# Optimization experiments

Measured on AMD Instinct MI355X. Metric: run time of the kernel, lower is better.

Reference implementation:

```python
import jax, jax.numpy as jnp
import numpy as np

B = 4096          # batch of samples
M = 128           # n_orbitals
F = 32            # n_fermions
H = 512           # hidden_units


def setup_inputs() -> dict:
    key = jax.random.key(0)
    kn, kphi, kw1, kb1, kw2, kb2 = jax.random.split(key, 6)
    # occupancy strings: exactly F ones among M orbitals per sample
    keys = jax.random.split(kn, B)
    occ_idx = jax.vmap(lambda k: jax.random.permutation(k, M)[:F])(keys)  # [B,F]
    n = jnp.zeros((B, M), jnp.float32).at[jnp.arange(B)[:, None], occ_idx].set(1.0)
    # parameters
    Phi = jax.random.normal(kphi, (F, M), jnp.float32) * 0.1
    W1 = jax.random.normal(kw1, (M, H), jnp.float32) / np.sqrt(M)
    b1 = jnp.zeros((H,), jnp.float32)
    W2 = jax.random.normal(kw2, (H, F * M), jnp.float32) / np.sqrt(H)
    b2 = jnp.zeros((F * M,), jnp.float32)
    return {"n": n, "Phi": Phi, "W1": W1, "b1": b1, "W2": W2, "b2": b2}


def reference(n, Phi, W1, b1, W2, b2):
    # backflow MLP: Dense -> tanh -> Dense, reshaped to (F, M) per sample
    h = jnp.tanh(n @ W1 + b1)                       # [B,H]
    bf = (h @ W2 + b2).reshape(-1, F, M)            # [B,F,M]
    kernel = Phi[None] + bf                         # [B,F,M]
    # occupied orbital columns; exactly F ones per row, top_k is stable so
    # indices come out in ascending order (same as jnp.where(n, size=F))
    idx = jax.lax.top_k(n, F)[1]                    # [B,F] int32
    phi = jnp.take_along_axis(kernel, idx[:, None, :], axis=2)  # [B,F,F]
    sign, logabs = jnp.linalg.slogdet(phi)
    return jnp.log(sign.astype(jnp.complex64)) + logabs.astype(jnp.complex64)  # [B] complex
```

## Files before the change

kernel.cpp:

```cpp
#include <hip/hip_runtime.h>
#include <hip/hip_bf16.h>
#include <math.h>

#define B_N 4096
#define M_N 128
#define F_N 32
#define H_N 512
#define NFM 4096

#define WAVE_SYNC() do { \
  asm volatile("s_waitcnt lgkmcnt(0)" ::: "memory"); \
  __builtin_amdgcn_sched_barrier(0); \
} while (0)

__global__ __launch_bounds__(256) void k1_idx_h(
    const float* __restrict__ n, const float* __restrict__ W1,
    const float* __restrict__ b1, float* __restrict__ h_ws,
    unsigned int* __restrict__ mask)
{
  __shared__ int s_idx[F_N];
  __shared__ int s_cnt0;
  const int b = blockIdx.x;
  const int t = threadIdx.x;

  bool p = false;
  int before = 0;
  if (t < 128) {
    float v = n[(size_t)b * M_N + t];
    p = v > 0.5f;
    unsigned long long m = __ballot(p);
    int lane = t & 63;
    before = __popcll(m & ((1ull << lane) - 1ull));
    if (lane == 0) {
      if (t < 64) { mask[b*4+0] = (unsigned)m; mask[b*4+1] = (unsigned)(m>>32); }
      else        { mask[b*4+2] = (unsigned)m; mask[b*4+3] = (unsigned)(m>>32); }
    }
    if (t < 64) {
      if (lane == 0) s_cnt0 = __popcll(m);
      if (p) s_idx[before] = t;
    }
  }
  __syncthreads();
  if (t >= 64 && t < 128 && p) s_idx[s_cnt0 + before] = t;
  __syncthreads();

  #pragma unroll
  for (int cc = 0; cc < 2; ++cc) {
    int c = t + cc * 256;
    float acc = 0.0f;
    #pragma unroll
    for (int j = 0; j < F_N; ++j)
      acc += W1[(size_t)s_idx[j] * H_N + c];
    acc += b1[c];
    h_ws[(size_t)b * H_N + c] = tanhf(acc);
  }
}

__global__ __launch_bounds__(256) void k_w2t(
    const float* __restrict__ W2, float* __restrict__ W2t)
{
  __shared__ float lds[32 * 132];
  const int k = blockIdx.x;
  const int t = threadIdx.x;

  #pragma unroll
  for (int i = 0; i < 4; ++i) {
    int m0 = i * 1024 + t * 4;
    float4 v = *(const float4*)&W2[(size_t)k * NFM + m0];
    int ig = m0 >> 7, c = m0 & 127;
    lds[ig * 132 + c + 0] = v.x;
    lds[ig * 132 + c + 1] = v.y;
    lds[ig * 132 + c + 2] = v.z;
    lds[ig * 132 + c + 3] = v.w;
  }
  __syncthreads();

  const int c  = t >> 1;
  const int ih = (t & 1) * 16;
  float* outp = W2t + (size_t)c * (H_N * F_N) + k * F_N + ih;
  #pragma unroll
  for (int i = 0; i < 4; ++i) {
    int ig = ih + i * 4;
    float4 v = make_float4(lds[(ig + 0) * 132 + c], lds[(ig + 1) * 132 + c],
                           lds[(ig + 2) * 132 + c], lds[(ig + 3) * 132 + c]);
    *(float4*)(outp + i * 4) = v;
  }
}

__global__ __launch_bounds__(256) void k_fill(
    const unsigned int* __restrict__ mask,
    int* __restrict__ bcnt, int* __restrict__ boff,
    int* __restrict__ bent, int* __restrict__ loc)
{
  const int c = blockIdx.x;
  const int t = threadIdx.x;
  const int w = t >> 6, lane = t & 63;
  const int word = c >> 5, bit = c & 31;
  __shared__ int s_wcnt[4];
  __shared__ int s_red[8];
  __shared__ int s_run;

  int cnt_loc = 0, off_loc = 0;
  for (int b = t; b < B_N; b += 256) {
    unsigned m0 = mask[(size_t)b*4+0], m1 = mask[(size_t)b*4+1];
    unsigned m2 = mask[(size_t)b*4+2], m3 = mask[(size_t)b*4+3];
    unsigned wv = (word == 0) ? m0 : (word == 1) ? m1 : (word == 2) ? m2 : m3;
    cnt_loc += (int)((wv >> bit) & 1u);
    int r = __popc(wv & ((1u << bit) - 1u));
    if (word > 0) r += __popc(m0);
    if (word > 1) r += __popc(m1);
    if (word > 2) r += __popc(m2);
    off_loc += r;
  }
  #pragma unroll
  for (int off = 32; off > 0; off >>= 1) {
    cnt_loc += __shfl_down(cnt_loc, off);
    off_loc += __shfl_down(off_loc, off);
  }
  if (lane == 0) { s_red[w] = cnt_loc; s_red[4 + w] = off_loc; }
  __syncthreads();
  const int cnt_tot = s_red[0] + s_red[1] + s_red[2] + s_red[3];
  const int off_tot = s_red[4] + s_red[5] + s_red[6] + s_red[7];
  if (t == 0) { bcnt[c] = cnt_tot; boff[c] = off_tot; s_run = 0; }
  __syncthreads();

  for (int chunk = 0; chunk < B_N; chunk += 256) {
    const int b = chunk + t;
    unsigned m0 = mask[(size_t)b*4+0], m1 = mask[(size_t)b*4+1];
    unsigned m2 = mask[(size_t)b*4+2], m3 = mask[(size_t)b*4+3];
    unsigned wv = (word == 0) ? m0 : (word == 1) ? m1 : (word == 2) ? m2 : m3;
    bool p = (wv >> bit) & 1u;
    int j = __popc(wv & ((1u << bit) - 1u));
    if (word > 0) j += __popc(m0);
    if (word > 1) j += __popc(m1);
    if (word > 2) j += __popc(m2);

    unsigned long long bal = __ballot(p);
    int before = __popcll(bal & ((1ull << lane) - 1ull));
    if (lane == 0) s_wcnt[w] = __popcll(bal);
    __syncthreads();
    int wbase = s_run;
    for (int i = 0; i < w; ++i) wbase += s_wcnt[i];
    if (p) {
      int pos = wbase + before;
      bent[(size_t)c * B_N + pos] = (b << 5) | j;
      loc[b * 32 + j] = off_tot + pos;
    }
    __syncthreads();
    if (t == 0) s_run += s_wcnt[0] + s_wcnt[1] + s_wcnt[2] + s_wcnt[3];
    __syncthreads();
  }
}

__global__ __launch_bounds__(256) void k2_gemm_gather(
    const float* __restrict__ h, const float* __restrict__ W2t,
    const float* __restrict__ b2, const float* __restrict__ Phi,
    const int* __restrict__ bcnt, const int* __restrict__ boff,
    const int* __restrict__ bent, float* __restrict__ phi_bucket)
{
  __shared__ __align__(16) float smem[2 * 2336];
  __shared__ int s_b[256];

  const int tid = threadIdx.x;
  const int c   = blockIdx.x;
  const int cnt = bcnt[c];
  const int t0  = blockIdx.y * 256;
  if (t0 >= cnt) return;
  const int base = boff[c];
  const float* w2tc = W2t + (size_t)c * (H_N * F_N);

  {
    int ii = t0 + tid;
    int e  = bent[(size_t)c * B_N + (ii < cnt ? ii : cnt - 1)];
    s_b[tid] = e >> 5;
  }
  __syncthreads();

  const int kA = tid & 7;
  const int ty = tid >> 3;
  const int tx = tid & 7;
  const int r8 = ty * 8;

  int rowb[8];
  #pragma unroll
  for (int i = 0; i < 8; ++i) rowb[i] = s_b[r8 + i];

  float acc[8][4];
  #pragma unroll
  for (int i = 0; i < 8; ++i)
    #pragma unroll
    for (int u = 0; u < 4; ++u) acc[i][u] = 0.f;

  float aReg[8], bReg;

  #pragma unroll
  for (int i = 0; i < 8; ++i)
    aReg[i] = h[(size_t)rowb[i] * H_N + kA];
  bReg = w2tc[tid];
  #pragma unroll
  for (int u = 0; u < 2; ++u)
    *(float4*)&smem[kA * 260 + r8 + u * 4] =
        make_float4(aReg[4*u], aReg[4*u+1], aReg[4*u+2], aReg[4*u+3]);
  smem[2080 + tid] = bReg;
  __syncthreads();

  #pragma unroll 1
  for (int t = 0; t < 64; ++t) {
    float* Atc = smem + (t & 1) * 2336;
    float* Btc = Atc + 2080;
    float* Atn = smem + ((t + 1) & 1) * 2336;
    float* Btn = Atn + 2080;

    if (t < 63) {
      int k0n = (t + 1) * 8;
      #pragma unroll
      for (int i = 0; i < 8; ++i)
        aReg[i] = h[(size_t)rowb[i] * H_N + k0n + kA];
      bReg = w2tc[k0n * 32 + tid];
    }

    #pragma unroll
    for (int kk = 0; kk < 8; ++kk) {
      float4 a0 = *(const float4*)&Atc[kk * 260 + r8];
      float4 a1 = *(const float4*)&Atc[kk * 260 + r8 + 4];
      float4 bv = *(const float4*)&Btc[kk * 32 + tx * 4];
      float a8[8] = {a0.x, a0.y, a0.z, a0.w, a1.x, a1.y, a1.z, a1.w};
      float b4[4] = {bv.x, bv.y, bv.z, bv.w};
      #pragma unroll
      for (int i = 0; i < 8; ++i)
        #pragma unroll
        for (int u = 0; u < 4; ++u)
          acc[i][u] = fmaf(a8[i], b4[u], acc[i][u]);
    }

    if (t < 63) {
      #pragma unroll
      for (int u = 0; u < 2; ++u)
        *(float4*)&Atn[kA * 260 + r8 + u * 4] =
            make_float4(aReg[4*u], aReg[4*u+1], aReg[4*u+2], aReg[4*u+3]);
      Btn[tid] = bReg;
      __syncthreads();
    }
  }

  float ph[4], bb[4];
  #pragma unroll
  for (int u = 0; u < 4; ++u) {
    int colw = (tx * 4 + u) * M_N + c;
    ph[u] = Phi[colw];
    bb[u] = b2[colw];
  }
  #pragma unroll
  for (int i = 0; i < 8; ++i) {
    int r = r8 + i;
    if (t0 + r < cnt) {
      int col = base + t0 + r;
      float v0 = ph[0] + (acc[i][0] + bb[0]);
      float v1 = ph[1] + (acc[i][1] + bb[1]);
      float v2 = ph[2] + (acc[i][2] + bb[2]);
      float v3 = ph[3] + (acc[i][3] + bb[3]);
      *(float4*)&phi_bucket[(size_t)col * 32 + tx * 4] =
          make_float4(v0, v1, v2, v3);
    }
  }
}

__global__ __launch_bounds__(256) void k3_det(
    const float* __restrict__ phi_bucket, const int* __restrict__ loc,
    float* __restrict__ out)
{
  __shared__ float A[4][32 * 33];
  const int w = threadIdx.x >> 6;
  const int lane = threadIdx.x & 63;
  const int b = blockIdx.x * 4 + w;
  float* Aw = A[w];

  {
    const int jj = lane & 31;
    const int hi = lane >> 5;
    int lcol = loc[b * 32 + jj];
    const float* colp = phi_bucket + (size_t)lcol * 32 + hi * 16;
    #pragma unroll
    for (int i = 0; i < 4; ++i) {
      float4 v = *(const float4*)(colp + i * 4);
      int ig = hi * 16 + i * 4;
      Aw[(ig + 0) * 33 + jj] = v.x;
      Aw[(ig + 1) * 33 + jj] = v.y;
      Aw[(ig + 2) * 33 + jj] = v.z;
      Aw[(ig + 3) * 33 + jj] = v.w;
    }
  }
  WAVE_SYNC();

  float logabs = 0.f;
  int negs = 0;
  for (int k = 0; k < 32; ++k) {
    float v = -1.f;
    int vi = lane;
    if (lane >= k && lane < 32) v = fabsf(Aw[lane * 33 + k]);
    #pragma unroll
    for (int off = 32; off > 0; off >>= 1) {
      float ov = __shfl_xor(v, off);
      int oi = __shfl_xor(vi, off);
      if (ov > v || (ov == v && oi < vi)) { v = ov; vi = oi; }
    }
    int p = vi;
    if (p != k) {
      negs ^= 1;
      if (lane < 32) {
        float tmp = Aw[k * 33 + lane];
        Aw[k * 33 + lane] = Aw[p * 33 + lane];
        Aw[p * 33 + lane] = tmp;
      }
    }
    WAVE_SYNC();
    float piv = Aw[k * 33 + k];
    if (piv < 0.f) negs ^= 1;
    logabs += logf(fabsf(piv));
    if (lane > k && lane < 32) {
      float l = Aw[lane * 33 + k];
      if (fabsf(piv) >= 1.17549435e-38f) l = l * (1.0f / piv);
      else                               l = l / piv;
      Aw[lane * 33 + k] = l;
    }
    WAVE_SYNC();
    {
      const int mid = (k + 33) >> 1;
      const int j   = lane & 31;
      const int ilo = (lane < 32) ? (k + 1) : mid;
      const int ihi = (lane < 32) ? mid : 32;
      if (j > k) {
        float nukj = -Aw[k * 33 + j];
        for (int i = ilo; i < ihi; ++i)
          Aw[i * 33 + j] = fmaf(nukj, Aw[i * 33 + k], Aw[i * 33 + j]);
      }
    }
    WAVE_SYNC();
  }

  if (lane == 0) {
    out[b]       = logabs;
    out[B_N + b] = (negs & 1) ? 3.14159265358979f : 0.0f;
  }
}

extern "C" void kernel_launch(void* const* d_in, const int* in_sizes, int n_in,
                              void* d_out, int out_size, void* d_ws, size_t ws_size,
                              hipStream_t stream) {
  const float* n   = (const float*)d_in[0];
  const float* Phi = (const float*)d_in[1];
  const float* W1  = (const float*)d_in[2];
  const float* b1  = (const float*)d_in[3];
  const float* W2  = (const float*)d_in[4];
  const float* b2  = (const float*)d_in[5];
  float* out = (float*)d_out;

  char* ws = (char*)d_ws;
  float*        h_ws       = (float*)ws;
  float*        phi_bucket = (float*)(ws + (size_t)8  * 1024 * 1024);
  float*        W2t        = (float*)(ws + (size_t)24 * 1024 * 1024);
  unsigned int* mask       = (unsigned int*)(ws + (size_t)32 * 1024 * 1024);
  int*          bent       = (int*)(ws + (size_t)32 * 1024 * 1024 + 65536);
  int*          loc        = (int*)(ws + (size_t)34 * 1024 * 1024 + 65536);
  int*          bcnt       = (int*)(ws + (size_t)34 * 1024 * 1024 + 65536 + 524288);
  int*          boff       = (int*)(ws + (size_t)34 * 1024 * 1024 + 65536 + 524288 + 4096);

  hipLaunchKernelGGL(k_w2t, dim3(H_N), dim3(256), 0, stream, W2, W2t);
  hipLaunchKernelGGL(k1_idx_h, dim3(B_N), dim3(256), 0, stream,
                     n, W1, b1, h_ws, mask);
  hipLaunchKernelGGL(k_fill, dim3(M_N), dim3(256), 0, stream,
                     mask, bcnt, boff, bent, loc);
  hipLaunchKernelGGL(k2_gemm_gather, dim3(M_N, 16), dim3(256), 0, stream,
                     h_ws, W2t, b2, Phi, bcnt, boff, bent, phi_bucket);
  hipLaunchKernelGGL(k3_det, dim3(B_N / 4), dim3(256), 0, stream,
                     phi_bucket, loc, out);
}
```

Before: 202.5 us.

## Replace LDS-staged gather GEMM with direct register-tiled global loads

The bucketed GEMM no longer stages h rows and W2t tiles in double-buffered shared memory. Each thread now loads float4 slices of its four h rows and the W2t column block straight from global memory into registers, double-buffered across k steps, and computes a 4x4 output tile. Rows per block drop from 256 to 128 and the grid doubles in y. This removes the LDS traffic and per-step barriers, but gives up shared-memory reuse, so it relies on L1/L2 to serve the redundant global loads of W2t and h.

```diff
diff --git a/kernel.cpp b/kernel.cpp
--- a/kernel.cpp
+++ b/kernel.cpp
@@ -152,95 +152,84 @@
   }
 }
 
+#define QK(A0,A1,A2,A3,C,BV) do { \
+  acc[0][0]=fmaf(A0.C,BV.x,acc[0][0]); acc[0][1]=fmaf(A0.C,BV.y,acc[0][1]); \
+  acc[0][2]=fmaf(A0.C,BV.z,acc[0][2]); acc[0][3]=fmaf(A0.C,BV.w,acc[0][3]); \
+  acc[1][0]=fmaf(A1.C,BV.x,acc[1][0]); acc[1][1]=fmaf(A1.C,BV.y,acc[1][1]); \
+  acc[1][2]=fmaf(A1.C,BV.z,acc[1][2]); acc[1][3]=fmaf(A1.C,BV.w,acc[1][3]); \
+  acc[2][0]=fmaf(A2.C,BV.x,acc[2][0]); acc[2][1]=fmaf(A2.C,BV.y,acc[2][1]); \
+  acc[2][2]=fmaf(A2.C,BV.z,acc[2][2]); acc[2][3]=fmaf(A2.C,BV.w,acc[2][3]); \
+  acc[3][0]=fmaf(A3.C,BV.x,acc[3][0]); acc[3][1]=fmaf(A3.C,BV.y,acc[3][1]); \
+  acc[3][2]=fmaf(A3.C,BV.z,acc[3][2]); acc[3][3]=fmaf(A3.C,BV.w,acc[3][3]); \
+} while(0)
+
+#define QUAD(A0,A1,A2,A3,B0,B1,B2,B3) do { \
+  QK(A0,A1,A2,A3,x,B0); QK(A0,A1,A2,A3,y,B1); \
+  QK(A0,A1,A2,A3,z,B2); QK(A0,A1,A2,A3,w,B3); \
+} while(0)
+
+#define LDQ(AA0,AA1,AA2,AA3,BB0,BB1,BB2,BB3,KOFF) do { \
+  AA0 = *(const float4*)(ap0 + (KOFF)); \
+  AA1 = *(const float4*)(ap1 + (KOFF)); \
+  AA2 = *(const float4*)(ap2 + (KOFF)); \
+  AA3 = *(const float4*)(ap3 + (KOFF)); \
+  BB0 = *(const float4*)(bp + (KOFF) * 32); \
+  BB1 = *(const float4*)(bp + (KOFF) * 32 + 32); \
+  BB2 = *(const float4*)(bp + (KOFF) * 32 + 64); \
+  BB3 = *(const float4*)(bp + (KOFF) * 32 + 96); \
+} while(0)
+
 __global__ __launch_bounds__(256) void k2_gemm_gather(
     const float* __restrict__ h, const float* __restrict__ W2t,
     const float* __restrict__ b2, const float* __restrict__ Phi,
     const int* __restrict__ bcnt, const int* __restrict__ boff,
     const int* __restrict__ bent, float* __restrict__ phi_bucket)
 {
-  __shared__ __align__(16) float smem[2 * 2336];
-  __shared__ int s_b[256];
+  __shared__ int s_b[128];
 
   const int tid = threadIdx.x;
   const int c   = blockIdx.x;
   const int cnt = bcnt[c];
-  const int t0  = blockIdx.y * 256;
+  const int t0  = blockIdx.y * 128;
   if (t0 >= cnt) return;
   const int base = boff[c];
   const float* w2tc = W2t + (size_t)c * (H_N * F_N);
 
-  {
+  if (tid < 128) {
     int ii = t0 + tid;
     int e  = bent[(size_t)c * B_N + (ii < cnt ? ii : cnt - 1)];
     s_b[tid] = e >> 5;
   }
   __syncthreads();
 
-  const int kA = tid & 7;
-  const int ty = tid >> 3;
-  const int tx = tid & 7;
-  const int r8 = ty * 8;
-
-  int rowb[8];
-  #pragma unroll
-  for (int i = 0; i < 8; ++i) rowb[i] = s_b[r8 + i];
-
-  float acc[8][4];
-  #pragma unroll
-  for (int i = 0; i < 8; ++i)
+  const int tx  = tid & 7;
+  const int tyr = tid >> 3;
+
+  const float* ap0 = h + (size_t)s_b[tyr * 4 + 0] * H_N;
+  const float* ap1 = h + (size_t)s_b[tyr * 4 + 1] * H_N;
+  const float* ap2 = h + (size_t)s_b[tyr * 4 + 2] * H_N;
+  const float* ap3 = h + (size_t)s_b[tyr * 4 + 3] * H_N;
+  const float* bp  = w2tc + tx * 4;
+
+  float acc[4][4];
+  #pragma unroll
+  for (int i = 0; i < 4; ++i)
     #pragma unroll
     for (int u = 0; u < 4; ++u) acc[i][u] = 0.f;
 
-  float aReg[8], bReg;
-
-  #pragma unroll
-  for (int i = 0; i < 8; ++i)
-    aReg[i] = h[(size_t)rowb[i] * H_N + kA];
-  bReg = w2tc[tid];
-  #pragma unroll
-  for (int u = 0; u < 2; ++u)
-    *(float4*)&smem[kA * 260 + r8 + u * 4] =
-        make_float4(aReg[4*u], aReg[4*u+1], aReg[4*u+2], aReg[4*u+3]);
-  smem[2080 + tid] = bReg;
-  __syncthreads();
+  float4 aA0, aA1, aA2, aA3, bA0, bA1, bA2, bA3;
+  float4 aB0, aB1, aB2, aB3, bB0, bB1, bB2, bB3;
+
+  LDQ(aA0, aA1, aA2, aA3, bA0, bA1, bA2, bA3, 0);
 
   #pragma unroll 1
-  for (int t = 0; t < 64; ++t) {
-    float* Atc = smem + (t & 1) * 2336;
-    float* Btc = Atc + 2080;
-    float* Atn = smem + ((t + 1) & 1) * 2336;
-    float* Btn = Atn + 2080;
-
-    if (t < 63) {
-      int k0n = (t + 1) * 8;
-      #pragma unroll
-      for (int i = 0; i < 8; ++i)
-        aReg[i] = h[(size_t)rowb[i] * H_N + k0n + kA];
-      bReg = w2tc[k0n * 32 + tid];
-    }
-
-    #pragma unroll
-    for (int kk = 0; kk < 8; ++kk) {
-      float4 a0 = *(const float4*)&Atc[kk * 260 + r8];
-      float4 a1 = *(const float4*)&Atc[kk * 260 + r8 + 4];
-      float4 bv = *(const float4*)&Btc[kk * 32 + tx * 4];
-      float a8[8] = {a0.x, a0.y, a0.z, a0.w, a1.x, a1.y, a1.z, a1.w};
-      float b4[4] = {bv.x, bv.y, bv.z, bv.w};
-      #pragma unroll
-      for (int i = 0; i < 8; ++i)
-        #pragma unroll
-        for (int u = 0; u < 4; ++u)
-          acc[i][u] = fmaf(a8[i], b4[u], acc[i][u]);
-    }
-
-    if (t < 63) {
-      #pragma unroll
-      for (int u = 0; u < 2; ++u)
-        *(float4*)&Atn[kA * 260 + r8 + u * 4] =
-            make_float4(aReg[4*u], aReg[4*u+1], aReg[4*u+2], aReg[4*u+3]);
-      Btn[tid] = bReg;
-      __syncthreads();
-    }
+  for (int kq = 0; kq < 64; ++kq) {
+    const int k0 = kq * 8;
+    LDQ(aB0, aB1, aB2, aB3, bB0, bB1, bB2, bB3, k0 + 4);
+    QUAD(aA0, aA1, aA2, aA3, bA0, bA1, bA2, bA3);
+    if (kq < 63)
+      LDQ(aA0, aA1, aA2, aA3, bA0, bA1, bA2, bA3, k0 + 8);
+    QUAD(aB0, aB1, aB2, aB3, bB0, bB1, bB2, bB3);
   }
 
   float ph[4], bb[4];
@@ -251,8 +240,8 @@
     bb[u] = b2[colw];
   }
   #pragma unroll
-  for (int i = 0; i < 8; ++i) {
-    int r = r8 + i;
+  for (int i = 0; i < 4; ++i) {
+    int r = tyr * 4 + i;
     if (t0 + r < cnt) {
       int col = base + t0 + r;
       float v0 = ph[0] + (acc[i][0] + bb[0]);
@@ -370,7 +359,7 @@
                      n, W1, b1, h_ws, mask);
   hipLaunchKernelGGL(k_fill, dim3(M_N), dim3(256), 0, stream,
                      mask, bcnt, boff, bent, loc);
-  hipLaunchKernelGGL(k2_gemm_gather, dim3(M_N, 16), dim3(256), 0, stream,
+  hipLaunchKernelGGL(k2_gemm_gather, dim3(M_N, 32), dim3(256), 0, stream,
                      h_ws, W2t, b2, Phi, bcnt, boff, bent, phi_bucket);
   hipLaunchKernelGGL(k3_det, dim3(B_N / 4), dim3(256), 0, stream,
                      phi_bucket, loc, out);
```

New measurement: 236.5 us. 16.8% more time.
